# Kernel tuning notes

Measured on AMD Instinct MI355X. Metric: run time of the kernel, lower is better.

Reference implementation:

```python
import jax, jax.numpy as jnp
import numpy as np

B, CIN, COUT, H, W = 64, 64, 64, 128, 128
M1, M2 = 32, 32


def _dht(x, s=None, axes=(-2, -1)):
    # Discrete Hartley Transform: real(FFT) - imag(FFT), norm='forward'
    f = jnp.fft.fftn(x, s=s, axes=axes, norm='forward')
    return jnp.real(f) - jnp.imag(f)


def setup_inputs() -> dict:
    key = jax.random.key(0)
    k1, k2, k3 = jax.random.split(key, 3)
    scale = 1.0 / (CIN * COUT)
    x = jax.random.normal(k1, (B, CIN, H, W), dtype=jnp.float32)
    weights1 = scale * jax.random.uniform(k2, (CIN, COUT, M1, M2), dtype=jnp.float32)
    weights2 = scale * jax.random.uniform(k3, (CIN, COUT, M1, M2), dtype=jnp.float32)
    return {"x": x, "weights1": weights1, "weights2": weights2}


def reference(x, weights1, weights2):
    b = x.shape[0]  # == CIN == COUT (required for the original torch.mul broadcast)
    # Full-grid DHT over spatial dims
    x_ft = _dht(x, axes=(2, 3))  # [B, CIN, H, W]

    def spectral_block(a, w):
        # convolution_using_DHT: DHT(a) * DHT(w), then inverse = (1/len) * DHT
        prod = _dht(a, axes=(-2, -1)) * _dht(w, axes=(-2, -1))  # [B, COUT, M1, M2]
        return (1.0 / b) * _dht(prod, axes=(-2, -1))  # len(prod) = b

    c1 = spectral_block(x_ft[:, :, :M1, :M2], weights1)
    c2 = spectral_block(x_ft[:, :, -M1:, :M2], weights2)

    # out_ft is cfloat in torch but only assigned real values -> keep real
    out_ft = jnp.zeros((b, COUT, H, W // 2 + 1), dtype=jnp.float32)
    out_ft = out_ft.at[:, :, :M1, :M2].set(c1)
    out_ft = out_ft.at[:, :, -M1:, :M2].set(c2)

    # InverseDHT with s=(H, W): zero-pads last dim from W//2+1 to W, scale 1/len
    return (1.0 / b) * _dht(out_ft, s=(H, W), axes=(2, 3))  # [B, COUT, H, W]
```

## Files before the change

kernel.cpp:

```cpp
#include <hip/hip_runtime.h>


#define OFF_T3   0
#define OFF_T4T  2048
#define OFF_TF   4096
#define OFF_XCY  53248
#define WS_FLOATS (53248 + 4096 * 2048)

typedef __attribute__((ext_vector_type(8))) short bf16x8;
typedef __attribute__((ext_vector_type(4))) float f32x4;

__device__ __forceinline__ int kmap(int i) { return (i < 32) ? i : 64 + i; }

__device__ __forceinline__ unsigned short f2bf(float f) {
    unsigned int u = __float_as_uint(f);
    return (unsigned short)((u + 0x7fffu + ((u >> 16) & 1u)) >> 16);
}
__device__ __forceinline__ float bf2f(unsigned short h) {
    return __uint_as_float(((unsigned int)h) << 16);
}

__device__ __forceinline__ void fma4(float* a, float s, float4 b) {
    a[0] = fmaf(s, b.x, a[0]); a[1] = fmaf(s, b.y, a[1]);
    a[2] = fmaf(s, b.z, a[2]); a[3] = fmaf(s, b.w, a[3]);
}

__global__ __launch_bounds__(256) void init_tables(float* ws) {
    int idx = blockIdx.x * 256 + threadIdx.x;
    if (idx >= 4096) return;
    const float w32 = 6.2831853071795864769f / 32.0f;
    if (idx < 2048) {
        int n2 = idx >> 6, j = idx & 63, jj = j & 31;
        float a = w32 * (float)((jj * n2) & 31);
        ws[OFF_T3 + idx] = (j < 32) ? cosf(a) : sinf(a);
    } else {
        int t = idx - 2048, m = t >> 5, k1 = t & 31;
        float v;
        if (m < 32) { float a = w32 * (float)((k1 * m) & 31); v = cosf(a) + sinf(a); }
        else { int mm = m - 32; float a = w32 * (float)((k1 * mm) & 31); v = cosf(a) - sinf(a); }
        ws[OFF_T4T + t] = v * (1.0f / 1024.0f);
    }
}

__global__ __launch_bounds__(256) void init_frag(float* ws) {
    unsigned short* tf = (unsigned short*)(ws + OFF_TF);
    int idx = blockIdx.x * 256 + threadIdx.x;
    if (idx >= 98304) return;
    const float w128 = 6.2831853071795864769f / 128.0f;
    float v;
    int hl;
    if (idx < 16384) {
        int frag = idx >> 9, lane = (idx >> 3) & 63, ii = idx & 7;
        hl = frag & 1;
        int nt = (frag >> 1) & 3, ks = frag >> 3;
        int n2 = ks * 32 + (lane >> 4) * 8 + ii;
        int j = nt * 16 + (lane & 15);
        int jj = j & 31;
        float a = w128 * (float)((jj * n2) & 127);
        v = (j < 32) ? cosf(a) : sinf(a);
    } else if (idx < 49152) {
        int t = idx - 16384;
        int frag = t >> 9, lane = (t >> 3) & 63, ii = t & 7;
        hl = frag & 1;
        int ks = (frag >> 1) & 7, mt = frag >> 4;
        int m = ks * 32 + (lane >> 4) * 8 + ii;
        int io = mt * 16 + (lane & 15);
        int k1 = kmap(io);
        if (m < 128) { float a = w128 * (float)((k1 * m) & 127); v = cosf(a) + sinf(a); }
        else { int mm = m - 128; float a = w128 * (float)((k1 * mm) & 127); v = cosf(a) - sinf(a); }
        v *= (1.0f / 16384.0f);
    } else if (idx < 81920) {
        int t = idx - 49152;
        int frag = t >> 9, lane = (t >> 3) & 63, ii = t & 7;
        hl = frag & 1;
        int nt = (frag >> 1) & 15, ks = frag >> 5;
        int j = ks * 32 + (lane >> 4) * 8 + ii;
        int r = nt * 16 + (lane & 15);
        int k1 = kmap(j);
        int p = r & 127;
        float a = w128 * (float)((p * k1) & 127);
        v = (r < 128) ? cosf(a) : sinf(a);
    } else {
        int t = idx - 81920;
        int frag = t >> 9, lane = (t >> 3) & 63, ii = t & 7;
        hl = frag & 1;
        int nt = (frag >> 1) & 7, ks = frag >> 4;
        int ms = ks * 32 + (lane >> 4) * 8 + ii;
        int q = nt * 16 + (lane & 15);
        int k2 = ms & 31;
        float a = w128 * (float)((q * k2) & 127);
        float c = cosf(a), s = sinf(a);
        const float s4 = 1.0f / 67108864.0f;
        v = ((ms < 32) ? (c + s) : (c - s)) * s4;
    }
    unsigned short h = f2bf(v);
    tf[idx] = hl ? f2bf(v - bf2f(h)) : h;
}

__global__ __launch_bounds__(256) void kA(const float* __restrict__ x, float* ws) {
    __shared__ unsigned short CSThi[64 * 136];
    __shared__ unsigned short CSTlo[64 * 136];
    const int tid  = threadIdx.x;
    const int lane = tid & 63;
    const int wv   = tid >> 6;
    const int ch   = blockIdx.x;
    const float* xg = x + ch * 16384;
    const int lr = lane & 15;
    const int lk = (lane >> 4) * 8;
    const int lq = (lane >> 4) * 4;

    const unsigned short* tf = (const unsigned short*)(ws + OFF_TF);
    const bf16x8* t1f = (const bf16x8*)tf;
    const bf16x8* t2f = (const bf16x8*)tf + 32 * 64;

    const f32x4 zero4 = {0.f, 0.f, 0.f, 0.f};

    f32x4 acc[2][4];
#pragma unroll
    for (int mt = 0; mt < 2; mt++)
#pragma unroll
        for (int nt = 0; nt < 4; nt++) acc[mt][nt] = zero4;

#pragma unroll
    for (int ks = 0; ks < 4; ks++) {
        bf16x8 ah[2], al[2];
#pragma unroll
        for (int mt = 0; mt < 2; mt++) {
            const float* src = xg + (wv * 32 + mt * 16 + lr) * 128 + ks * 32 + lk;
            float4 u0 = *(const float4*)src;
            float4 u1 = *(const float4*)(src + 4);
            float av[8] = {u0.x, u0.y, u0.z, u0.w, u1.x, u1.y, u1.z, u1.w};
#pragma unroll
            for (int i = 0; i < 8; i++) {
                unsigned short h = f2bf(av[i]);
                ah[mt][i] = (short)h;
                al[mt][i] = (short)f2bf(av[i] - bf2f(h));
            }
        }
#pragma unroll
        for (int nt = 0; nt < 4; nt++) {
            bf16x8 bh = t1f[((ks * 4 + nt) * 2 + 0) * 64 + lane];
            bf16x8 bl = t1f[((ks * 4 + nt) * 2 + 1) * 64 + lane];
#pragma unroll
            for (int mt = 0; mt < 2; mt++) {
                acc[mt][nt] = __builtin_amdgcn_mfma_f32_16x16x32_bf16(ah[mt], bh, acc[mt][nt], 0, 0, 0);
                acc[mt][nt] = __builtin_amdgcn_mfma_f32_16x16x32_bf16(ah[mt], bl, acc[mt][nt], 0, 0, 0);
                acc[mt][nt] = __builtin_amdgcn_mfma_f32_16x16x32_bf16(al[mt], bh, acc[mt][nt], 0, 0, 0);
            }
        }
    }

#pragma unroll
    for (int mt = 0; mt < 2; mt++)
#pragma unroll
        for (int nt = 0; nt < 4; nt++) {
            const int j  = nt * 16 + lr;
            const int n1 = wv * 32 + mt * 16 + lq;
            unsigned short h[4], lo[4];
#pragma unroll
            for (int r = 0; r < 4; r++) {
                float v = acc[mt][nt][r];
                h[r]  = f2bf(v);
                lo[r] = f2bf(v - bf2f(h[r]));
            }
            uint2 hv = make_uint2((unsigned int)h[0] | ((unsigned int)h[1] << 16),
                                  (unsigned int)h[2] | ((unsigned int)h[3] << 16));
            uint2 lv = make_uint2((unsigned int)lo[0] | ((unsigned int)lo[1] << 16),
                                  (unsigned int)lo[2] | ((unsigned int)lo[3] << 16));
            *(uint2*)&CSThi[j * 136 + n1] = hv;
            *(uint2*)&CSTlo[j * 136 + n1] = lv;
        }
    __syncthreads();

    f32x4 a2[2] = {zero4, zero4};
#pragma unroll
    for (int ks = 0; ks < 8; ks++) {
        bf16x8 ah = t2f[((wv * 8 + ks) * 2 + 0) * 64 + lane];
        bf16x8 al = t2f[((wv * 8 + ks) * 2 + 1) * 64 + lane];
        const int colb = (ks & 3) * 32 + lk;
        const int rofs = (ks >= 4) ? 32 : 0;
#pragma unroll
        for (int nt = 0; nt < 2; nt++) {
            const int row = nt * 16 + lr + rofs;
            bf16x8 bh = *(const bf16x8*)&CSThi[row * 136 + colb];
            bf16x8 bl = *(const bf16x8*)&CSTlo[row * 136 + colb];
            a2[nt] = __builtin_amdgcn_mfma_f32_16x16x32_bf16(ah, bh, a2[nt], 0, 0, 0);
            a2[nt] = __builtin_amdgcn_mfma_f32_16x16x32_bf16(ah, bl, a2[nt], 0, 0, 0);
            a2[nt] = __builtin_amdgcn_mfma_f32_16x16x32_bf16(al, bh, a2[nt], 0, 0, 0);
        }
    }
    float* xcg = ws + OFF_XCY + ch * 2048;
#pragma unroll
    for (int nt = 0; nt < 2; nt++)
#pragma unroll
        for (int r = 0; r < 4; r++) {
            const int io = wv * 16 + lq + r;
            xcg[io * 32 + nt * 16 + lr] = a2[nt][r];
        }
}

__global__ __launch_bounds__(128) void kB1(const float* __restrict__ w1, const float* __restrict__ w2,
                                           float* ws, float* wh) {
    __shared__ float inT[2304];
    __shared__ float G[4352];
    __shared__ float T3c[2048];
    __shared__ float T4c[2048];
    const int tid = threadIdx.x;
#pragma unroll
    for (int i = 0; i < 16; i++) {
        int t = i * 128 + tid;
        T3c[t] = ws[OFF_T3 + t];
        T4c[t] = ws[OFF_T4T + t];
    }
    float* dstp[2];
#pragma unroll
    for (int tt = 0; tt < 2; tt++) {
        int g = blockIdx.x * 2 + tt;
        const float* src; float* dst;
        if (g < 8192) {
            int ch = g >> 1, crop = g & 1;
            dst = ws + OFF_XCY + ch * 2048 + crop * 1024;
            src = dst;
        } else {
            int gw = g - 8192;
            int ch = gw >> 1, t2 = gw & 1;
            src = (t2 ? w2 : w1) + ch * 1024;
            dst = wh + gw * 1024;
        }
        dstp[tt] = dst;
#pragma unroll
        for (int i = 0; i < 8; i++) {
            int idx = i * 128 + tid;
            int rr = idx >> 5, cc = idx & 31;
            inT[tt * 1152 + cc * 36 + rr] = src[idx];
        }
    }
    __syncthreads();
    {
        const int tt = tid >> 6, l = tid & 63;
        const int n10 = (l >> 4) * 8;
        const int jj0 = (l & 15) * 4;
        float ac[8][4];
#pragma unroll
        for (int i = 0; i < 8; i++) { ac[i][0] = ac[i][1] = ac[i][2] = ac[i][3] = 0.f; }
#pragma unroll 4
        for (int k = 0; k < 32; k++) {
            float4 b  = *(const float4*)&T3c[k * 64 + jj0];
            float4 a0 = *(const float4*)&inT[tt * 1152 + k * 36 + n10];
            float4 a1 = *(const float4*)&inT[tt * 1152 + k * 36 + n10 + 4];
            fma4(ac[0], a0.x, b); fma4(ac[1], a0.y, b);
            fma4(ac[2], a0.z, b); fma4(ac[3], a0.w, b);
            fma4(ac[4], a1.x, b); fma4(ac[5], a1.y, b);
            fma4(ac[6], a1.z, b); fma4(ac[7], a1.w, b);
        }
#pragma unroll
        for (int i = 0; i < 8; i++)
            *(float4*)&G[tt * 2176 + (n10 + i) * 68 + jj0] =
                make_float4(ac[i][0], ac[i][1], ac[i][2], ac[i][3]);
    }
    __syncthreads();
    {
        const int tt = tid >> 6, l = tid & 63;
        const int k10 = (l >> 3) * 4;
        const int k20 = (l & 7) * 4;
        float ac[4][4];
#pragma unroll
        for (int i = 0; i < 4; i++) { ac[i][0] = ac[i][1] = ac[i][2] = ac[i][3] = 0.f; }
#pragma unroll 4
        for (int m = 0; m < 64; m++) {
            float4 av = *(const float4*)&T4c[m * 32 + k10];
            const int row = m & 31;
            const int col = (m < 32) ? k20 : (32 + k20);
            float4 bv = *(const float4*)&G[tt * 2176 + row * 68 + col];
            fma4(ac[0], av.x, bv); fma4(ac[1], av.y, bv);
            fma4(ac[2], av.z, bv); fma4(ac[3], av.w, bv);
        }
        float* dst = dstp[tt];
#pragma unroll
        for (int i = 0; i < 4; i++)
            *(float4*)&dst[(k10 + i) * 32 + k20] =
                make_float4(ac[i][0], ac[i][1], ac[i][2], ac[i][3]);
    }
}

__global__ __launch_bounds__(128) void kB2(float* ws, const float* __restrict__ wh) {
    __shared__ float prodT[2304];
    __shared__ float G[4352];
    __shared__ float T3c[2048];
    __shared__ float T4c[2048];
    const int tid = threadIdx.x;
    const int ch = blockIdx.x;
#pragma unroll
    for (int i = 0; i < 16; i++) {
        int t = i * 128 + tid;
        T3c[t] = ws[OFF_T3 + t];
        T4c[t] = ws[OFF_T4T + t];
    }
    float* xc = ws + OFF_XCY + ch * 2048;
    const float* whc = wh + ch * 2048;
#pragma unroll
    for (int i = 0; i < 16; i++) {
        int flat = i * 128 + tid;
        int c = flat >> 10, r = (flat >> 5) & 31, cc = flat & 31;
        prodT[c * 1152 + cc * 36 + r] = xc[flat] * whc[flat];
    }
    __syncthreads();
    {
        const int tt = tid >> 6, l = tid & 63;
        const int n10 = (l >> 4) * 8;
        const int jj0 = (l & 15) * 4;
        float ac[8][4];
#pragma unroll
        for (int i = 0; i < 8; i++) { ac[i][0] = ac[i][1] = ac[i][2] = ac[i][3] = 0.f; }
#pragma unroll 4
        for (int k = 0; k < 32; k++) {
            float4 b  = *(const float4*)&T3c[k * 64 + jj0];
            float4 a0 = *(const float4*)&prodT[tt * 1152 + k * 36 + n10];
            float4 a1 = *(const float4*)&prodT[tt * 1152 + k * 36 + n10 + 4];
            fma4(ac[0], a0.x, b); fma4(ac[1], a0.y, b);
            fma4(ac[2], a0.z, b); fma4(ac[3], a0.w, b);
            fma4(ac[4], a1.x, b); fma4(ac[5], a1.y, b);
            fma4(ac[6], a1.z, b); fma4(ac[7], a1.w, b);
        }
#pragma unroll
        for (int i = 0; i < 8; i++)
            *(float4*)&G[tt * 2176 + (n10 + i) * 68 + jj0] =
                make_float4(ac[i][0], ac[i][1], ac[i][2], ac[i][3]);
    }
    __syncthreads();
    {
        const int tt = tid >> 6, l = tid & 63;
        const int k10 = (l >> 3) * 4;
        const int k20 = (l & 7) * 4;
        float ac[4][4];
#pragma unroll
        for (int i = 0; i < 4; i++) { ac[i][0] = ac[i][1] = ac[i][2] = ac[i][3] = 0.f; }
#pragma unroll 4
        for (int m = 0; m < 64; m++) {
            float4 av = *(const float4*)&T4c[m * 32 + k10];
            const int row = m & 31;
            const int col = (m < 32) ? k20 : (32 + k20);
            float4 bv = *(const float4*)&G[tt * 2176 + row * 68 + col];
            fma4(ac[0], av.x, bv); fma4(ac[1], av.y, bv);
            fma4(ac[2], av.z, bv); fma4(ac[3], av.w, bv);
        }
        float* dst = xc + tt * 1024;
#pragma unroll
        for (int i = 0; i < 4; i++)
            *(float4*)&dst[(k10 + i) * 32 + k20] =
                make_float4(ac[i][0], ac[i][1], ac[i][2], ac[i][3]);
    }
}

__global__ __launch_bounds__(256) void kC(float* __restrict__ out, float* ws) {
    __shared__ unsigned short YThi[32 * 72];
    __shared__ unsigned short YTlo[32 * 72];
    __shared__ unsigned short WThi[128 * 72];
    __shared__ unsigned short WTlo[128 * 72];
    const int tid  = threadIdx.x;
    const int lane = tid & 63;
    const int wv   = tid >> 6;
    const int ch   = blockIdx.x;
    const int lr = lane & 15;
    const int lk = (lane >> 4) * 8;
    const int lq = (lane >> 4) * 4;
    const float* yg = ws + OFF_XCY + ch * 2048;

    const unsigned short* tf = (const unsigned short*)(ws + OFF_TF);
    const bf16x8* t5f = (const bf16x8*)tf + 6144;
    const bf16x8* t6f = (const bf16x8*)tf + 10240;

    const f32x4 zero4 = {0.f, 0.f, 0.f, 0.f};

    {
        const int base = tid * 8;
        const int j = base >> 5, k2b = base & 31;
        float4 u0 = *(const float4*)&yg[base];
        float4 u1 = *(const float4*)&yg[base + 4];
        float av[8] = {u0.x, u0.y, u0.z, u0.w, u1.x, u1.y, u1.z, u1.w};
#pragma unroll
        for (int i = 0; i < 8; i++) {
            unsigned short h = f2bf(av[i]);
            YThi[(k2b + i) * 72 + j] = h;
            YTlo[(k2b + i) * 72 + j] = f2bf(av[i] - bf2f(h));
        }
    }
    __syncthreads();

    f32x4 acc1[2][4];
#pragma unroll
    for (int mt = 0; mt < 2; mt++)
#pragma unroll
        for (int n = 0; n < 4; n++) acc1[mt][n] = zero4;
    bf16x8 yh[2][2], yl[2][2];
#pragma unroll
    for (int mt = 0; mt < 2; mt++)
#pragma unroll
        for (int ks = 0; ks < 2; ks++) {
            yh[mt][ks] = *(const bf16x8*)&YThi[(mt * 16 + lr) * 72 + ks * 32 + lk];
            yl[mt][ks] = *(const bf16x8*)&YTlo[(mt * 16 + lr) * 72 + ks * 32 + lk];
        }
#pragma unroll
    for (int ks = 0; ks < 2; ks++)
#pragma unroll
        for (int ntl = 0; ntl < 4; ntl++) {
            const int nt = wv * 4 + ntl;
            bf16x8 bh = t5f[((ks * 16 + nt) * 2 + 0) * 64 + lane];
            bf16x8 bl = t5f[((ks * 16 + nt) * 2 + 1) * 64 + lane];
#pragma unroll
            for (int mt = 0; mt < 2; mt++) {
                acc1[mt][ntl] = __builtin_amdgcn_mfma_f32_16x16x32_bf16(yh[mt][ks], bh, acc1[mt][ntl], 0, 0, 0);
                acc1[mt][ntl] = __builtin_amdgcn_mfma_f32_16x16x32_bf16(yh[mt][ks], bl, acc1[mt][ntl], 0, 0, 0);
                acc1[mt][ntl] = __builtin_amdgcn_mfma_f32_16x16x32_bf16(yl[mt][ks], bh, acc1[mt][ntl], 0, 0, 0);
            }
        }

#pragma unroll
    for (int mt = 0; mt < 2; mt++)
#pragma unroll
        for (int ntl = 0; ntl < 4; ntl++) {
            const int nt = wv * 4 + ntl;
            const int p = (nt & 7) * 16 + lr;
            const int ms0 = ((nt >= 8) ? 32 : 0) + mt * 16 + lq;
            unsigned short h[4], lo[4];
#pragma unroll
            for (int r = 0; r < 4; r++) {
                float v = acc1[mt][ntl][r];
                h[r]  = f2bf(v);
                lo[r] = f2bf(v - bf2f(h[r]));
            }
            *(uint2*)&WThi[p * 72 + ms0] =
                make_uint2((unsigned int)h[0] | ((unsigned int)h[1] << 16),
                           (unsigned int)h[2] | ((unsigned int)h[3] << 16));
            *(uint2*)&WTlo[p * 72 + ms0] =
                make_uint2((unsigned int)lo[0] | ((unsigned int)lo[1] << 16),
                           (unsigned int)lo[2] | ((unsigned int)lo[3] << 16));
        }
    __syncthreads();

    bf16x8 wth[2][2], wtl[2][2];
#pragma unroll
    for (int mtl = 0; mtl < 2; mtl++)
#pragma unroll
        for (int ks = 0; ks < 2; ks++) {
            const int row = (wv * 2 + mtl) * 16 + lr;
            wth[mtl][ks] = *(const bf16x8*)&WThi[row * 72 + ks * 32 + lk];
            wtl[mtl][ks] = *(const bf16x8*)&WTlo[row * 72 + ks * 32 + lk];
        }
    f32x4 acc2[2][8];
#pragma unroll
    for (int mtl = 0; mtl < 2; mtl++)
#pragma unroll
        for (int n = 0; n < 8; n++) acc2[mtl][n] = zero4;
#pragma unroll
    for (int ks = 0; ks < 2; ks++)
#pragma unroll
        for (int nt = 0; nt < 8; nt++) {
            bf16x8 bh = t6f[((ks * 8 + nt) * 2 + 0) * 64 + lane];
            bf16x8 bl = t6f[((ks * 8 + nt) * 2 + 1) * 64 + lane];
#pragma unroll
            for (int mtl = 0; mtl < 2; mtl++) {
                acc2[mtl][nt] = __builtin_amdgcn_mfma_f32_16x16x32_bf16(wth[mtl][ks], bh, acc2[mtl][nt], 0, 0, 0);
                acc2[mtl][nt] = __builtin_amdgcn_mfma_f32_16x16x32_bf16(wth[mtl][ks], bl, acc2[mtl][nt], 0, 0, 0);
                acc2[mtl][nt] = __builtin_amdgcn_mfma_f32_16x16x32_bf16(wtl[mtl][ks], bh, acc2[mtl][nt], 0, 0, 0);
            }
        }
    float* og = out + ch * 16384;
#pragma unroll
    for (int mtl = 0; mtl < 2; mtl++) {
        const int pb = (wv * 2 + mtl) * 16 + lq;
#pragma unroll
        for (int nt = 0; nt < 8; nt++)
#pragma unroll
            for (int r = 0; r < 4; r++)
                og[(pb + r) * 128 + nt * 16 + lr] = acc2[mtl][nt][r];
    }
}

extern "C" void kernel_launch(void* const* d_in, const int* in_sizes, int n_in,
                              void* d_out, int out_size, void* d_ws, size_t ws_size,
                              hipStream_t stream) {
    (void)in_sizes; (void)n_in; (void)out_size;
    if (ws_size < (size_t)WS_FLOATS * sizeof(float)) return;
    const float* x  = (const float*)d_in[0];
    const float* w1 = (const float*)d_in[1];
    const float* w2 = (const float*)d_in[2];
    float* out = (float*)d_out;
    float* ws  = (float*)d_ws;
    float* wh  = out;

    hipLaunchKernelGGL(init_tables, dim3(16), dim3(256), 0, stream, ws);
    hipLaunchKernelGGL(init_frag, dim3(384), dim3(256), 0, stream, ws);
    hipLaunchKernelGGL(kA,  dim3(4096), dim3(256), 0, stream, x, ws);
    hipLaunchKernelGGL(kB1, dim3(8192), dim3(128), 0, stream, w1, w2, ws, wh);
    hipLaunchKernelGGL(kB2, dim3(4096), dim3(128), 0, stream, ws, wh);
    hipLaunchKernelGGL(kC,  dim3(4096), dim3(256), 0, stream, out, ws);
}
```

Before: 635.6 us.

## Fuse all spectral stages into a single per-channel kernel with MFMA 32-point DHTs

Merges the separate forward-DHT, small 32x32 spectral-block, and inverse-DHT kernels into one kernel per channel that keeps intermediates in shared memory. The fp32 CUDA-core 32-point transforms are replaced by split-bf16 MFMA matmuls using new precomputed fragment tables. This removes the large global workspace round-trip and several launches, at the cost of higher shared memory use (60KB per block), which may lower occupancy.

```diff
diff --git a/kernel.cpp b/kernel.cpp
--- a/kernel.cpp
+++ b/kernel.cpp
@@ -1,11 +1,7 @@
 #include <hip/hip_runtime.h>
 
 
-#define OFF_T3   0
-#define OFF_T4T  2048
-#define OFF_TF   4096
-#define OFF_XCY  53248
-#define WS_FLOATS (53248 + 4096 * 2048)
+#define WS_FLOATS 53248
 
 typedef __attribute__((ext_vector_type(8))) short bf16x8;
 typedef __attribute__((ext_vector_type(4))) float f32x4;
@@ -20,33 +16,25 @@
     return __uint_as_float(((unsigned int)h) << 16);
 }
 
-__device__ __forceinline__ void fma4(float* a, float s, float4 b) {
-    a[0] = fmaf(s, b.x, a[0]); a[1] = fmaf(s, b.y, a[1]);
-    a[2] = fmaf(s, b.z, a[2]); a[3] = fmaf(s, b.w, a[3]);
-}
-
-__global__ __launch_bounds__(256) void init_tables(float* ws) {
+__device__ __forceinline__ void pack4(f32x4 v, uint2* hv, uint2* lv) {
+    unsigned short h[4], lo[4];
+#pragma unroll
+    for (int r = 0; r < 4; r++) {
+        h[r]  = f2bf(v[r]);
+        lo[r] = f2bf(v[r] - bf2f(h[r]));
+    }
+    *hv = make_uint2((unsigned int)h[0] | ((unsigned int)h[1] << 16),
+                     (unsigned int)h[2] | ((unsigned int)h[3] << 16));
+    *lv = make_uint2((unsigned int)lo[0] | ((unsigned int)lo[1] << 16),
+                     (unsigned int)lo[2] | ((unsigned int)lo[3] << 16));
+}
+
+__global__ __launch_bounds__(256) void init_frag(float* ws) {
+    unsigned short* tf = (unsigned short*)ws;
     int idx = blockIdx.x * 256 + threadIdx.x;
-    if (idx >= 4096) return;
-    const float w32 = 6.2831853071795864769f / 32.0f;
-    if (idx < 2048) {
-        int n2 = idx >> 6, j = idx & 63, jj = j & 31;
-        float a = w32 * (float)((jj * n2) & 31);
-        ws[OFF_T3 + idx] = (j < 32) ? cosf(a) : sinf(a);
-    } else {
-        int t = idx - 2048, m = t >> 5, k1 = t & 31;
-        float v;
-        if (m < 32) { float a = w32 * (float)((k1 * m) & 31); v = cosf(a) + sinf(a); }
-        else { int mm = m - 32; float a = w32 * (float)((k1 * mm) & 31); v = cosf(a) - sinf(a); }
-        ws[OFF_T4T + t] = v * (1.0f / 1024.0f);
-    }
-}
-
-__global__ __launch_bounds__(256) void init_frag(float* ws) {
-    unsigned short* tf = (unsigned short*)(ws + OFF_TF);
-    int idx = blockIdx.x * 256 + threadIdx.x;
-    if (idx >= 98304) return;
+    if (idx >= 106496) return;
     const float w128 = 6.2831853071795864769f / 128.0f;
+    const float w32  = 6.2831853071795864769f / 32.0f;
     float v;
     int hl;
     if (idx < 16384) {
@@ -80,7 +68,7 @@
         int p = r & 127;
         float a = w128 * (float)((p * k1) & 127);
         v = (r < 128) ? cosf(a) : sinf(a);
-    } else {
+    } else if (idx < 98304) {
         int t = idx - 81920;
         int frag = t >> 9, lane = (t >> 3) & 63, ii = t & 7;
         hl = frag & 1;
@@ -92,84 +80,107 @@
         float c = cosf(a), s = sinf(a);
         const float s4 = 1.0f / 67108864.0f;
         v = ((ms < 32) ? (c + s) : (c - s)) * s4;
+    } else if (idx < 102400) {
+        int t = idx - 98304;
+        int frag = t >> 9, lane = (t >> 3) & 63, ii = t & 7;
+        hl = frag & 1;
+        int nt = frag >> 1;
+        int k = (lane >> 4) * 8 + ii;
+        int j = nt * 16 + (lane & 15);
+        int jj = j & 31;
+        float a = w32 * (float)((jj * k) & 31);
+        v = (j < 32) ? cosf(a) : sinf(a);
+    } else {
+        int t = idx - 102400;
+        int frag = t >> 9, lane = (t >> 3) & 63, ii = t & 7;
+        hl = frag & 1;
+        int ks = (frag >> 1) & 1, mt = frag >> 2;
+        int m = ks * 32 + (lane >> 4) * 8 + ii;
+        int k1 = mt * 16 + (lane & 15);
+        if (m < 32) { float a = w32 * (float)((k1 * m) & 31); v = cosf(a) + sinf(a); }
+        else { int mm = m - 32; float a = w32 * (float)((k1 * mm) & 31); v = cosf(a) - sinf(a); }
+        v *= (1.0f / 1024.0f);
     }
     unsigned short h = f2bf(v);
     tf[idx] = hl ? f2bf(v - bf2f(h)) : h;
 }
 
-__global__ __launch_bounds__(256) void kA(const float* __restrict__ x, float* ws) {
-    __shared__ unsigned short CSThi[64 * 136];
-    __shared__ unsigned short CSTlo[64 * 136];
+__global__ __launch_bounds__(256) void kFused(const float* __restrict__ x,
+                                              const float* __restrict__ w1,
+                                              const float* __restrict__ w2,
+                                              float* __restrict__ out,
+                                              const float* __restrict__ ws) {
+    __shared__ __align__(16) unsigned char smem[61440];
     const int tid  = threadIdx.x;
     const int lane = tid & 63;
     const int wv   = tid >> 6;
     const int ch   = blockIdx.x;
-    const float* xg = x + ch * 16384;
     const int lr = lane & 15;
     const int lk = (lane >> 4) * 8;
     const int lq = (lane >> 4) * 4;
-
-    const unsigned short* tf = (const unsigned short*)(ws + OFF_TF);
-    const bf16x8* t1f = (const bf16x8*)tf;
-    const bf16x8* t2f = (const bf16x8*)tf + 32 * 64;
+    const float* xg = x + ch * 16384;
+
+    const bf16x8* tfv = (const bf16x8*)ws;
+    const bf16x8* t1f = tfv;
+    const bf16x8* t2f = tfv + 32 * 64;
+    const bf16x8* t5f = tfv + 96 * 64;
+    const bf16x8* t6f = tfv + 160 * 64;
+    const bf16x8* t3f = tfv + 192 * 64;
+    const bf16x8* t4f = tfv + 200 * 64;
+
+    float4 wl1 = *(const float4*)(w1 + ch * 1024 + tid * 4);
+    float4 wl2 = *(const float4*)(w2 + ch * 1024 + tid * 4);
 
     const f32x4 zero4 = {0.f, 0.f, 0.f, 0.f};
 
-    f32x4 acc[2][4];
-#pragma unroll
-    for (int mt = 0; mt < 2; mt++)
-#pragma unroll
-        for (int nt = 0; nt < 4; nt++) acc[mt][nt] = zero4;
-
-#pragma unroll
-    for (int ks = 0; ks < 4; ks++) {
-        bf16x8 ah[2], al[2];
-#pragma unroll
-        for (int mt = 0; mt < 2; mt++) {
-            const float* src = xg + (wv * 32 + mt * 16 + lr) * 128 + ks * 32 + lk;
-            float4 u0 = *(const float4*)src;
-            float4 u1 = *(const float4*)(src + 4);
-            float av[8] = {u0.x, u0.y, u0.z, u0.w, u1.x, u1.y, u1.z, u1.w};
-#pragma unroll
-            for (int i = 0; i < 8; i++) {
-                unsigned short h = f2bf(av[i]);
-                ah[mt][i] = (short)h;
-                al[mt][i] = (short)f2bf(av[i] - bf2f(h));
-            }
-        }
-#pragma unroll
-        for (int nt = 0; nt < 4; nt++) {
-            bf16x8 bh = t1f[((ks * 4 + nt) * 2 + 0) * 64 + lane];
-            bf16x8 bl = t1f[((ks * 4 + nt) * 2 + 1) * 64 + lane];
+    unsigned short* CSThi = (unsigned short*)smem;
+    unsigned short* CSTlo = (unsigned short*)(smem + 17408);
+    {
+        f32x4 acc[2][4];
+#pragma unroll
+        for (int mt = 0; mt < 2; mt++)
+#pragma unroll
+            for (int nt = 0; nt < 4; nt++) acc[mt][nt] = zero4;
+#pragma unroll
+        for (int ks = 0; ks < 4; ks++) {
+            bf16x8 ah[2], al[2];
 #pragma unroll
             for (int mt = 0; mt < 2; mt++) {
-                acc[mt][nt] = __builtin_amdgcn_mfma_f32_16x16x32_bf16(ah[mt], bh, acc[mt][nt], 0, 0, 0);
-                acc[mt][nt] = __builtin_amdgcn_mfma_f32_16x16x32_bf16(ah[mt], bl, acc[mt][nt], 0, 0, 0);
-                acc[mt][nt] = __builtin_amdgcn_mfma_f32_16x16x32_bf16(al[mt], bh, acc[mt][nt], 0, 0, 0);
-            }
-        }
-    }
-
-#pragma unroll
-    for (int mt = 0; mt < 2; mt++)
-#pragma unroll
-        for (int nt = 0; nt < 4; nt++) {
-            const int j  = nt * 16 + lr;
-            const int n1 = wv * 32 + mt * 16 + lq;
-            unsigned short h[4], lo[4];
-#pragma unroll
-            for (int r = 0; r < 4; r++) {
-                float v = acc[mt][nt][r];
-                h[r]  = f2bf(v);
-                lo[r] = f2bf(v - bf2f(h[r]));
-            }
-            uint2 hv = make_uint2((unsigned int)h[0] | ((unsigned int)h[1] << 16),
-                                  (unsigned int)h[2] | ((unsigned int)h[3] << 16));
-            uint2 lv = make_uint2((unsigned int)lo[0] | ((unsigned int)lo[1] << 16),
-                                  (unsigned int)lo[2] | ((unsigned int)lo[3] << 16));
-            *(uint2*)&CSThi[j * 136 + n1] = hv;
-            *(uint2*)&CSTlo[j * 136 + n1] = lv;
-        }
+                const float* src = xg + (wv * 32 + mt * 16 + lr) * 128 + ks * 32 + lk;
+                float4 u0 = *(const float4*)src;
+                float4 u1 = *(const float4*)(src + 4);
+                float av[8] = {u0.x, u0.y, u0.z, u0.w, u1.x, u1.y, u1.z, u1.w};
+#pragma unroll
+                for (int i = 0; i < 8; i++) {
+                    unsigned short h = f2bf(av[i]);
+                    ah[mt][i] = (short)h;
+                    al[mt][i] = (short)f2bf(av[i] - bf2f(h));
+                }
+            }
+#pragma unroll
+            for (int nt = 0; nt < 4; nt++) {
+                bf16x8 bh = t1f[((ks * 4 + nt) * 2 + 0) * 64 + lane];
+                bf16x8 bl = t1f[((ks * 4 + nt) * 2 + 1) * 64 + lane];
+#pragma unroll
+                for (int mt = 0; mt < 2; mt++) {
+                    acc[mt][nt] = __builtin_amdgcn_mfma_f32_16x16x32_bf16(ah[mt], bh, acc[mt][nt], 0, 0, 0);
+                    acc[mt][nt] = __builtin_amdgcn_mfma_f32_16x16x32_bf16(ah[mt], bl, acc[mt][nt], 0, 0, 0);
+                    acc[mt][nt] = __builtin_amdgcn_mfma_f32_16x16x32_bf16(al[mt], bh, acc[mt][nt], 0, 0, 0);
+                }
+            }
+        }
+#pragma unroll
+        for (int mt = 0; mt < 2; mt++)
+#pragma unroll
+            for (int nt = 0; nt < 4; nt++) {
+                const int j  = nt * 16 + lr;
+                const int n1 = wv * 32 + mt * 16 + lq;
+                uint2 hv, lv;
+                pack4(acc[mt][nt], &hv, &lv);
+                *(uint2*)&CSThi[j * 136 + n1] = hv;
+                *(uint2*)&CSTlo[j * 136 + n1] = lv;
+            }
+    }
     __syncthreads();
 
     f32x4 a2[2] = {zero4, zero4};
@@ -189,291 +200,277 @@
             a2[nt] = __builtin_amdgcn_mfma_f32_16x16x32_bf16(al, bh, a2[nt], 0, 0, 0);
         }
     }
-    float* xcg = ws + OFF_XCY + ch * 2048;
-#pragma unroll
-    for (int nt = 0; nt < 2; nt++)
-#pragma unroll
-        for (int r = 0; r < 4; r++) {
-            const int io = wv * 16 + lq + r;
-            xcg[io * 32 + nt * 16 + lr] = a2[nt][r];
-        }
-}
-
-__global__ __launch_bounds__(128) void kB1(const float* __restrict__ w1, const float* __restrict__ w2,
-                                           float* ws, float* wh) {
-    __shared__ float inT[2304];
-    __shared__ float G[4352];
-    __shared__ float T3c[2048];
-    __shared__ float T4c[2048];
-    const int tid = threadIdx.x;
-#pragma unroll
-    for (int i = 0; i < 16; i++) {
-        int t = i * 128 + tid;
-        T3c[t] = ws[OFF_T3 + t];
-        T4c[t] = ws[OFF_T4T + t];
-    }
-    float* dstp[2];
-#pragma unroll
-    for (int tt = 0; tt < 2; tt++) {
-        int g = blockIdx.x * 2 + tt;
-        const float* src; float* dst;
-        if (g < 8192) {
-            int ch = g >> 1, crop = g & 1;
-            dst = ws + OFF_XCY + ch * 2048 + crop * 1024;
-            src = dst;
-        } else {
-            int gw = g - 8192;
-            int ch = gw >> 1, t2 = gw & 1;
-            src = (t2 ? w2 : w1) + ch * 1024;
-            dst = wh + gw * 1024;
-        }
-        dstp[tt] = dst;
+    __syncthreads();
+
+    unsigned short* XCFhi = (unsigned short*)smem;
+    unsigned short* XCFlo = (unsigned short*)(smem + 10240);
+    {
+        const int c  = wv >> 1;
+        const int nb = (wv & 1) * 16 + lq;
+#pragma unroll
+        for (int nt = 0; nt < 2; nt++)
+#pragma unroll
+            for (int r = 0; r < 4; r++) {
+                float v = a2[nt][r];
+                unsigned short h = f2bf(v);
+                XCFhi[c * 1280 + (nb + r) * 40 + nt * 16 + lr] = h;
+                XCFlo[c * 1280 + (nb + r) * 40 + nt * 16 + lr] = f2bf(v - bf2f(h));
+            }
+        const int rw = tid >> 3, cw = (tid & 7) * 4;
+        float a1v[4] = {wl1.x, wl1.y, wl1.z, wl1.w};
+        float a2v[4] = {wl2.x, wl2.y, wl2.z, wl2.w};
+        unsigned short h1[4], l1[4], h2[4], l2[4];
+#pragma unroll
+        for (int i = 0; i < 4; i++) {
+            h1[i] = f2bf(a1v[i]); l1[i] = f2bf(a1v[i] - bf2f(h1[i]));
+            h2[i] = f2bf(a2v[i]); l2[i] = f2bf(a2v[i] - bf2f(h2[i]));
+        }
+        *(uint2*)&XCFhi[2 * 1280 + rw * 40 + cw] =
+            make_uint2((unsigned int)h1[0] | ((unsigned int)h1[1] << 16),
+                       (unsigned int)h1[2] | ((unsigned int)h1[3] << 16));
+        *(uint2*)&XCFlo[2 * 1280 + rw * 40 + cw] =
+            make_uint2((unsigned int)l1[0] | ((unsigned int)l1[1] << 16),
+                       (unsigned int)l1[2] | ((unsigned int)l1[3] << 16));
+        *(uint2*)&XCFhi[3 * 1280 + rw * 40 + cw] =
+            make_uint2((unsigned int)h2[0] | ((unsigned int)h2[1] << 16),
+                       (unsigned int)h2[2] | ((unsigned int)h2[3] << 16));
+        *(uint2*)&XCFlo[3 * 1280 + rw * 40 + cw] =
+            make_uint2((unsigned int)l2[0] | ((unsigned int)l2[1] << 16),
+                       (unsigned int)l2[2] | ((unsigned int)l2[3] << 16));
+    }
+    __syncthreads();
+
+    unsigned short* GThi = (unsigned short*)(smem + 20480);
+    unsigned short* GTlo = (unsigned short*)(smem + 40960);
+    {
+        const int t = wv;
+        f32x4 g[2][4];
+#pragma unroll
+        for (int mt = 0; mt < 2; mt++)
+#pragma unroll
+            for (int nt = 0; nt < 4; nt++) g[mt][nt] = zero4;
+        bf16x8 ah[2], al[2];
+#pragma unroll
+        for (int mt = 0; mt < 2; mt++) {
+            ah[mt] = *(const bf16x8*)&XCFhi[t * 1280 + (mt * 16 + lr) * 40 + lk];
+            al[mt] = *(const bf16x8*)&XCFlo[t * 1280 + (mt * 16 + lr) * 40 + lk];
+        }
+#pragma unroll
+        for (int nt = 0; nt < 4; nt++) {
+            bf16x8 bh = t3f[(nt * 2 + 0) * 64 + lane];
+            bf16x8 bl = t3f[(nt * 2 + 1) * 64 + lane];
+#pragma unroll
+            for (int mt = 0; mt < 2; mt++) {
+                g[mt][nt] = __builtin_amdgcn_mfma_f32_16x16x32_bf16(ah[mt], bh, g[mt][nt], 0, 0, 0);
+                g[mt][nt] = __builtin_amdgcn_mfma_f32_16x16x32_bf16(ah[mt], bl, g[mt][nt], 0, 0, 0);
+                g[mt][nt] = __builtin_amdgcn_mfma_f32_16x16x32_bf16(al[mt], bh, g[mt][nt], 0, 0, 0);
+            }
+        }
+#pragma unroll
+        for (int mt = 0; mt < 2; mt++)
+#pragma unroll
+            for (int nt = 0; nt < 4; nt++) {
+                const int j = nt * 16 + lr, n1b = mt * 16 + lq;
+                uint2 hv, lv;
+                pack4(g[mt][nt], &hv, &lv);
+                *(uint2*)&GThi[t * 2560 + j * 40 + n1b] = hv;
+                *(uint2*)&GTlo[t * 2560 + j * 40 + n1b] = lv;
+            }
+    }
+    __syncthreads();
+
+    float* HAT = (float*)smem;
+    {
+        const int t = wv;
+        f32x4 hacc[2][2];
+#pragma unroll
+        for (int mt = 0; mt < 2; mt++)
+#pragma unroll
+            for (int nt = 0; nt < 2; nt++) hacc[mt][nt] = zero4;
+#pragma unroll
+        for (int ks = 0; ks < 2; ks++) {
+#pragma unroll
+            for (int mt = 0; mt < 2; mt++) {
+                bf16x8 ah = t4f[((mt * 2 + ks) * 2 + 0) * 64 + lane];
+                bf16x8 al = t4f[((mt * 2 + ks) * 2 + 1) * 64 + lane];
+#pragma unroll
+                for (int nt = 0; nt < 2; nt++) {
+                    const int row = nt * 16 + lr + 32 * ks;
+                    bf16x8 bh = *(const bf16x8*)&GThi[t * 2560 + row * 40 + lk];
+                    bf16x8 bl = *(const bf16x8*)&GTlo[t * 2560 + row * 40 + lk];
+                    hacc[mt][nt] = __builtin_amdgcn_mfma_f32_16x16x32_bf16(ah, bh, hacc[mt][nt], 0, 0, 0);
+                    hacc[mt][nt] = __builtin_amdgcn_mfma_f32_16x16x32_bf16(ah, bl, hacc[mt][nt], 0, 0, 0);
+                    hacc[mt][nt] = __builtin_amdgcn_mfma_f32_16x16x32_bf16(al, bh, hacc[mt][nt], 0, 0, 0);
+                }
+            }
+        }
+        __syncthreads();
+#pragma unroll
+        for (int mt = 0; mt < 2; mt++)
+#pragma unroll
+            for (int nt = 0; nt < 2; nt++)
+#pragma unroll
+                for (int r = 0; r < 4; r++)
+                    HAT[t * 1152 + (mt * 16 + lq + r) * 36 + nt * 16 + lr] = hacc[mt][nt][r];
+    }
+    __syncthreads();
+
+    unsigned short* GT2hi = (unsigned short*)(smem + 20480);
+    unsigned short* GT2lo = (unsigned short*)(smem + 30720);
+    {
+        const int t = wv >> 1, h = wv & 1;
+        const int n1 = h * 16 + lr;
+        float pv[8];
 #pragma unroll
         for (int i = 0; i < 8; i++) {
-            int idx = i * 128 + tid;
-            int rr = idx >> 5, cc = idx & 31;
-            inT[tt * 1152 + cc * 36 + rr] = src[idx];
-        }
-    }
-    __syncthreads();
-    {
-        const int tt = tid >> 6, l = tid & 63;
-        const int n10 = (l >> 4) * 8;
-        const int jj0 = (l & 15) * 4;
-        float ac[8][4];
-#pragma unroll
-        for (int i = 0; i < 8; i++) { ac[i][0] = ac[i][1] = ac[i][2] = ac[i][3] = 0.f; }
-#pragma unroll 4
-        for (int k = 0; k < 32; k++) {
-            float4 b  = *(const float4*)&T3c[k * 64 + jj0];
-            float4 a0 = *(const float4*)&inT[tt * 1152 + k * 36 + n10];
-            float4 a1 = *(const float4*)&inT[tt * 1152 + k * 36 + n10 + 4];
-            fma4(ac[0], a0.x, b); fma4(ac[1], a0.y, b);
-            fma4(ac[2], a0.z, b); fma4(ac[3], a0.w, b);
-            fma4(ac[4], a1.x, b); fma4(ac[5], a1.y, b);
-            fma4(ac[6], a1.z, b); fma4(ac[7], a1.w, b);
-        }
-#pragma unroll
-        for (int i = 0; i < 8; i++)
-            *(float4*)&G[tt * 2176 + (n10 + i) * 68 + jj0] =
-                make_float4(ac[i][0], ac[i][1], ac[i][2], ac[i][3]);
-    }
-    __syncthreads();
-    {
-        const int tt = tid >> 6, l = tid & 63;
-        const int k10 = (l >> 3) * 4;
-        const int k20 = (l & 7) * 4;
-        float ac[4][4];
-#pragma unroll
-        for (int i = 0; i < 4; i++) { ac[i][0] = ac[i][1] = ac[i][2] = ac[i][3] = 0.f; }
-#pragma unroll 4
-        for (int m = 0; m < 64; m++) {
-            float4 av = *(const float4*)&T4c[m * 32 + k10];
-            const int row = m & 31;
-            const int col = (m < 32) ? k20 : (32 + k20);
-            float4 bv = *(const float4*)&G[tt * 2176 + row * 68 + col];
-            fma4(ac[0], av.x, bv); fma4(ac[1], av.y, bv);
-            fma4(ac[2], av.z, bv); fma4(ac[3], av.w, bv);
-        }
-        float* dst = dstp[tt];
-#pragma unroll
-        for (int i = 0; i < 4; i++)
-            *(float4*)&dst[(k10 + i) * 32 + k20] =
-                make_float4(ac[i][0], ac[i][1], ac[i][2], ac[i][3]);
-    }
-}
-
-__global__ __launch_bounds__(128) void kB2(float* ws, const float* __restrict__ wh) {
-    __shared__ float prodT[2304];
-    __shared__ float G[4352];
-    __shared__ float T3c[2048];
-    __shared__ float T4c[2048];
-    const int tid = threadIdx.x;
-    const int ch = blockIdx.x;
-#pragma unroll
-    for (int i = 0; i < 16; i++) {
-        int t = i * 128 + tid;
-        T3c[t] = ws[OFF_T3 + t];
-        T4c[t] = ws[OFF_T4T + t];
-    }
-    float* xc = ws + OFF_XCY + ch * 2048;
-    const float* whc = wh + ch * 2048;
-#pragma unroll
-    for (int i = 0; i < 16; i++) {
-        int flat = i * 128 + tid;
-        int c = flat >> 10, r = (flat >> 5) & 31, cc = flat & 31;
-        prodT[c * 1152 + cc * 36 + r] = xc[flat] * whc[flat];
-    }
-    __syncthreads();
-    {
-        const int tt = tid >> 6, l = tid & 63;
-        const int n10 = (l >> 4) * 8;
-        const int jj0 = (l & 15) * 4;
-        float ac[8][4];
-#pragma unroll
-        for (int i = 0; i < 8; i++) { ac[i][0] = ac[i][1] = ac[i][2] = ac[i][3] = 0.f; }
-#pragma unroll 4
-        for (int k = 0; k < 32; k++) {
-            float4 b  = *(const float4*)&T3c[k * 64 + jj0];
-            float4 a0 = *(const float4*)&prodT[tt * 1152 + k * 36 + n10];
-            float4 a1 = *(const float4*)&prodT[tt * 1152 + k * 36 + n10 + 4];
-            fma4(ac[0], a0.x, b); fma4(ac[1], a0.y, b);
-            fma4(ac[2], a0.z, b); fma4(ac[3], a0.w, b);
-            fma4(ac[4], a1.x, b); fma4(ac[5], a1.y, b);
-            fma4(ac[6], a1.z, b); fma4(ac[7], a1.w, b);
-        }
-#pragma unroll
-        for (int i = 0; i < 8; i++)
-            *(float4*)&G[tt * 2176 + (n10 + i) * 68 + jj0] =
-                make_float4(ac[i][0], ac[i][1], ac[i][2], ac[i][3]);
-    }
-    __syncthreads();
-    {
-        const int tt = tid >> 6, l = tid & 63;
-        const int k10 = (l >> 3) * 4;
-        const int k20 = (l & 7) * 4;
-        float ac[4][4];
-#pragma unroll
-        for (int i = 0; i < 4; i++) { ac[i][0] = ac[i][1] = ac[i][2] = ac[i][3] = 0.f; }
-#pragma unroll 4
-        for (int m = 0; m < 64; m++) {
-            float4 av = *(const float4*)&T4c[m * 32 + k10];
-            const int row = m & 31;
-            const int col = (m < 32) ? k20 : (32 + k20);
-            float4 bv = *(const float4*)&G[tt * 2176 + row * 68 + col];
-            fma4(ac[0], av.x, bv); fma4(ac[1], av.y, bv);
-            fma4(ac[2], av.z, bv); fma4(ac[3], av.w, bv);
-        }
-        float* dst = xc + tt * 1024;
-#pragma unroll
-        for (int i = 0; i < 4; i++)
-            *(float4*)&dst[(k10 + i) * 32 + k20] =
-                make_float4(ac[i][0], ac[i][1], ac[i][2], ac[i][3]);
-    }
-}
-
-__global__ __launch_bounds__(256) void kC(float* __restrict__ out, float* ws) {
-    __shared__ unsigned short YThi[32 * 72];
-    __shared__ unsigned short YTlo[32 * 72];
-    __shared__ unsigned short WThi[128 * 72];
-    __shared__ unsigned short WTlo[128 * 72];
-    const int tid  = threadIdx.x;
-    const int lane = tid & 63;
-    const int wv   = tid >> 6;
-    const int ch   = blockIdx.x;
-    const int lr = lane & 15;
-    const int lk = (lane >> 4) * 8;
-    const int lq = (lane >> 4) * 4;
-    const float* yg = ws + OFF_XCY + ch * 2048;
-
-    const unsigned short* tf = (const unsigned short*)(ws + OFF_TF);
-    const bf16x8* t5f = (const bf16x8*)tf + 6144;
-    const bf16x8* t6f = (const bf16x8*)tf + 10240;
-
-    const f32x4 zero4 = {0.f, 0.f, 0.f, 0.f};
-
-    {
-        const int base = tid * 8;
-        const int j = base >> 5, k2b = base & 31;
-        float4 u0 = *(const float4*)&yg[base];
-        float4 u1 = *(const float4*)&yg[base + 4];
-        float av[8] = {u0.x, u0.y, u0.z, u0.w, u1.x, u1.y, u1.z, u1.w};
+            float px = HAT[t * 1152 + n1 * 36 + lk + i];
+            float pw = HAT[(t + 2) * 1152 + n1 * 36 + lk + i];
+            pv[i] = px * pw;
+        }
+        bf16x8 ah, al;
 #pragma unroll
         for (int i = 0; i < 8; i++) {
-            unsigned short h = f2bf(av[i]);
-            YThi[(k2b + i) * 72 + j] = h;
-            YTlo[(k2b + i) * 72 + j] = f2bf(av[i] - bf2f(h));
-        }
-    }
-    __syncthreads();
-
-    f32x4 acc1[2][4];
-#pragma unroll
-    for (int mt = 0; mt < 2; mt++)
-#pragma unroll
-        for (int n = 0; n < 4; n++) acc1[mt][n] = zero4;
-    bf16x8 yh[2][2], yl[2][2];
-#pragma unroll
-    for (int mt = 0; mt < 2; mt++)
+            unsigned short hh = f2bf(pv[i]);
+            ah[i] = (short)hh;
+            al[i] = (short)f2bf(pv[i] - bf2f(hh));
+        }
+        f32x4 g[4];
+#pragma unroll
+        for (int nt = 0; nt < 4; nt++) g[nt] = zero4;
+#pragma unroll
+        for (int nt = 0; nt < 4; nt++) {
+            bf16x8 bh = t3f[(nt * 2 + 0) * 64 + lane];
+            bf16x8 bl = t3f[(nt * 2 + 1) * 64 + lane];
+            g[nt] = __builtin_amdgcn_mfma_f32_16x16x32_bf16(ah, bh, g[nt], 0, 0, 0);
+            g[nt] = __builtin_amdgcn_mfma_f32_16x16x32_bf16(ah, bl, g[nt], 0, 0, 0);
+            g[nt] = __builtin_amdgcn_mfma_f32_16x16x32_bf16(al, bh, g[nt], 0, 0, 0);
+        }
+#pragma unroll
+        for (int nt = 0; nt < 4; nt++) {
+            const int j = nt * 16 + lr, n1b = h * 16 + lq;
+            uint2 hv, lv;
+            pack4(g[nt], &hv, &lv);
+            *(uint2*)&GT2hi[t * 2560 + j * 40 + n1b] = hv;
+            *(uint2*)&GT2lo[t * 2560 + j * 40 + n1b] = lv;
+        }
+    }
+    __syncthreads();
+
+    unsigned short* YThi = (unsigned short*)smem;
+    unsigned short* YTlo = (unsigned short*)(smem + 4608);
+    {
+        const int t = wv >> 1, h = wv & 1;
+        f32x4 ya[2] = {zero4, zero4};
 #pragma unroll
         for (int ks = 0; ks < 2; ks++) {
-            yh[mt][ks] = *(const bf16x8*)&YThi[(mt * 16 + lr) * 72 + ks * 32 + lk];
-            yl[mt][ks] = *(const bf16x8*)&YTlo[(mt * 16 + lr) * 72 + ks * 32 + lk];
-        }
-#pragma unroll
-    for (int ks = 0; ks < 2; ks++)
-#pragma unroll
-        for (int ntl = 0; ntl < 4; ntl++) {
-            const int nt = wv * 4 + ntl;
-            bf16x8 bh = t5f[((ks * 16 + nt) * 2 + 0) * 64 + lane];
-            bf16x8 bl = t5f[((ks * 16 + nt) * 2 + 1) * 64 + lane];
-#pragma unroll
-            for (int mt = 0; mt < 2; mt++) {
-                acc1[mt][ntl] = __builtin_amdgcn_mfma_f32_16x16x32_bf16(yh[mt][ks], bh, acc1[mt][ntl], 0, 0, 0);
-                acc1[mt][ntl] = __builtin_amdgcn_mfma_f32_16x16x32_bf16(yh[mt][ks], bl, acc1[mt][ntl], 0, 0, 0);
-                acc1[mt][ntl] = __builtin_amdgcn_mfma_f32_16x16x32_bf16(yl[mt][ks], bh, acc1[mt][ntl], 0, 0, 0);
-            }
-        }
-
-#pragma unroll
-    for (int mt = 0; mt < 2; mt++)
-#pragma unroll
-        for (int ntl = 0; ntl < 4; ntl++) {
-            const int nt = wv * 4 + ntl;
-            const int p = (nt & 7) * 16 + lr;
-            const int ms0 = ((nt >= 8) ? 32 : 0) + mt * 16 + lq;
-            unsigned short h[4], lo[4];
-#pragma unroll
-            for (int r = 0; r < 4; r++) {
-                float v = acc1[mt][ntl][r];
-                h[r]  = f2bf(v);
-                lo[r] = f2bf(v - bf2f(h[r]));
-            }
-            *(uint2*)&WThi[p * 72 + ms0] =
-                make_uint2((unsigned int)h[0] | ((unsigned int)h[1] << 16),
-                           (unsigned int)h[2] | ((unsigned int)h[3] << 16));
-            *(uint2*)&WTlo[p * 72 + ms0] =
-                make_uint2((unsigned int)lo[0] | ((unsigned int)lo[1] << 16),
-                           (unsigned int)lo[2] | ((unsigned int)lo[3] << 16));
-        }
-    __syncthreads();
-
-    bf16x8 wth[2][2], wtl[2][2];
-#pragma unroll
-    for (int mtl = 0; mtl < 2; mtl++)
-#pragma unroll
-        for (int ks = 0; ks < 2; ks++) {
-            const int row = (wv * 2 + mtl) * 16 + lr;
-            wth[mtl][ks] = *(const bf16x8*)&WThi[row * 72 + ks * 32 + lk];
-            wtl[mtl][ks] = *(const bf16x8*)&WTlo[row * 72 + ks * 32 + lk];
-        }
-    f32x4 acc2[2][8];
-#pragma unroll
-    for (int mtl = 0; mtl < 2; mtl++)
-#pragma unroll
-        for (int n = 0; n < 8; n++) acc2[mtl][n] = zero4;
-#pragma unroll
-    for (int ks = 0; ks < 2; ks++)
-#pragma unroll
-        for (int nt = 0; nt < 8; nt++) {
-            bf16x8 bh = t6f[((ks * 8 + nt) * 2 + 0) * 64 + lane];
-            bf16x8 bl = t6f[((ks * 8 + nt) * 2 + 1) * 64 + lane];
-#pragma unroll
-            for (int mtl = 0; mtl < 2; mtl++) {
-                acc2[mtl][nt] = __builtin_amdgcn_mfma_f32_16x16x32_bf16(wth[mtl][ks], bh, acc2[mtl][nt], 0, 0, 0);
-                acc2[mtl][nt] = __builtin_amdgcn_mfma_f32_16x16x32_bf16(wth[mtl][ks], bl, acc2[mtl][nt], 0, 0, 0);
-                acc2[mtl][nt] = __builtin_amdgcn_mfma_f32_16x16x32_bf16(wtl[mtl][ks], bh, acc2[mtl][nt], 0, 0, 0);
-            }
-        }
-    float* og = out + ch * 16384;
-#pragma unroll
-    for (int mtl = 0; mtl < 2; mtl++) {
-        const int pb = (wv * 2 + mtl) * 16 + lq;
-#pragma unroll
-        for (int nt = 0; nt < 8; nt++)
-#pragma unroll
-            for (int r = 0; r < 4; r++)
-                og[(pb + r) * 128 + nt * 16 + lr] = acc2[mtl][nt][r];
+            bf16x8 ah = t4f[((h * 2 + ks) * 2 + 0) * 64 + lane];
+            bf16x8 al = t4f[((h * 2 + ks) * 2 + 1) * 64 + lane];
+#pragma unroll
+            for (int nt = 0; nt < 2; nt++) {
+                const int row = nt * 16 + lr + 32 * ks;
+                bf16x8 bh = *(const bf16x8*)&GT2hi[t * 2560 + row * 40 + lk];
+                bf16x8 bl = *(const bf16x8*)&GT2lo[t * 2560 + row * 40 + lk];
+                ya[nt] = __builtin_amdgcn_mfma_f32_16x16x32_bf16(ah, bh, ya[nt], 0, 0, 0);
+                ya[nt] = __builtin_amdgcn_mfma_f32_16x16x32_bf16(ah, bl, ya[nt], 0, 0, 0);
+                ya[nt] = __builtin_amdgcn_mfma_f32_16x16x32_bf16(al, bh, ya[nt], 0, 0, 0);
+            }
+        }
+        __syncthreads();
+#pragma unroll
+        for (int nt = 0; nt < 2; nt++) {
+            const int k2 = nt * 16 + lr;
+            const int j0 = t * 32 + h * 16 + lq;
+            uint2 hv, lv;
+            pack4(ya[nt], &hv, &lv);
+            *(uint2*)&YThi[k2 * 72 + j0] = hv;
+            *(uint2*)&YTlo[k2 * 72 + j0] = lv;
+        }
+    }
+    __syncthreads();
+
+    unsigned short* WThi = (unsigned short*)(smem + 9216);
+    unsigned short* WTlo = (unsigned short*)(smem + 27648);
+    {
+        f32x4 acc1[2][4];
+#pragma unroll
+        for (int mt = 0; mt < 2; mt++)
+#pragma unroll
+            for (int n = 0; n < 4; n++) acc1[mt][n] = zero4;
+        bf16x8 yh[2][2], yl[2][2];
+#pragma unroll
+        for (int mt = 0; mt < 2; mt++)
+#pragma unroll
+            for (int ks = 0; ks < 2; ks++) {
+                yh[mt][ks] = *(const bf16x8*)&YThi[(mt * 16 + lr) * 72 + ks * 32 + lk];
+                yl[mt][ks] = *(const bf16x8*)&YTlo[(mt * 16 + lr) * 72 + ks * 32 + lk];
+            }
+#pragma unroll
+        for (int ks = 0; ks < 2; ks++)
+#pragma unroll
+            for (int ntl = 0; ntl < 4; ntl++) {
+                const int nt = wv * 4 + ntl;
+                bf16x8 bh = t5f[((ks * 16 + nt) * 2 + 0) * 64 + lane];
+                bf16x8 bl = t5f[((ks * 16 + nt) * 2 + 1) * 64 + lane];
+#pragma unroll
+                for (int mt = 0; mt < 2; mt++) {
+                    acc1[mt][ntl] = __builtin_amdgcn_mfma_f32_16x16x32_bf16(yh[mt][ks], bh, acc1[mt][ntl], 0, 0, 0);
+                    acc1[mt][ntl] = __builtin_amdgcn_mfma_f32_16x16x32_bf16(yh[mt][ks], bl, acc1[mt][ntl], 0, 0, 0);
+                    acc1[mt][ntl] = __builtin_amdgcn_mfma_f32_16x16x32_bf16(yl[mt][ks], bh, acc1[mt][ntl], 0, 0, 0);
+                }
+            }
+#pragma unroll
+        for (int mt = 0; mt < 2; mt++)
+#pragma unroll
+            for (int ntl = 0; ntl < 4; ntl++) {
+                const int nt = wv * 4 + ntl;
+                const int p = (nt & 7) * 16 + lr;
+                const int ms0 = ((nt >= 8) ? 32 : 0) + mt * 16 + lq;
+                uint2 hv, lv;
+                pack4(acc1[mt][ntl], &hv, &lv);
+                *(uint2*)&WThi[p * 72 + ms0] = hv;
+                *(uint2*)&WTlo[p * 72 + ms0] = lv;
+            }
+    }
+    __syncthreads();
+
+    {
+        bf16x8 wth[2][2], wtl[2][2];
+#pragma unroll
+        for (int mtl = 0; mtl < 2; mtl++)
+#pragma unroll
+            for (int ks = 0; ks < 2; ks++) {
+                const int row = (wv * 2 + mtl) * 16 + lr;
+                wth[mtl][ks] = *(const bf16x8*)&WThi[row * 72 + ks * 32 + lk];
+                wtl[mtl][ks] = *(const bf16x8*)&WTlo[row * 72 + ks * 32 + lk];
+            }
+        f32x4 acc2[2][8];
+#pragma unroll
+        for (int mtl = 0; mtl < 2; mtl++)
+#pragma unroll
+            for (int n = 0; n < 8; n++) acc2[mtl][n] = zero4;
+#pragma unroll
+        for (int ks = 0; ks < 2; ks++)
+#pragma unroll
+            for (int nt = 0; nt < 8; nt++) {
+                bf16x8 bh = t6f[((ks * 8 + nt) * 2 + 0) * 64 + lane];
+                bf16x8 bl = t6f[((ks * 8 + nt) * 2 + 1) * 64 + lane];
+#pragma unroll
+                for (int mtl = 0; mtl < 2; mtl++) {
+                    acc2[mtl][nt] = __builtin_amdgcn_mfma_f32_16x16x32_bf16(wth[mtl][ks], bh, acc2[mtl][nt], 0, 0, 0);
+                    acc2[mtl][nt] = __builtin_amdgcn_mfma_f32_16x16x32_bf16(wth[mtl][ks], bl, acc2[mtl][nt], 0, 0, 0);
+                    acc2[mtl][nt] = __builtin_amdgcn_mfma_f32_16x16x32_bf16(wtl[mtl][ks], bh, acc2[mtl][nt], 0, 0, 0);
+                }
+            }
+        float* og = out + ch * 16384;
+#pragma unroll
+        for (int mtl = 0; mtl < 2; mtl++) {
+            const int pb = (wv * 2 + mtl) * 16 + lq;
+#pragma unroll
+            for (int nt = 0; nt < 8; nt++)
+#pragma unroll
+                for (int r = 0; r < 4; r++)
+                    og[(pb + r) * 128 + nt * 16 + lr] = acc2[mtl][nt][r];
+        }
     }
 }
 
@@ -487,12 +484,7 @@
     const float* w2 = (const float*)d_in[2];
     float* out = (float*)d_out;
     float* ws  = (float*)d_ws;
-    float* wh  = out;
-
-    hipLaunchKernelGGL(init_tables, dim3(16), dim3(256), 0, stream, ws);
-    hipLaunchKernelGGL(init_frag, dim3(384), dim3(256), 0, stream, ws);
-    hipLaunchKernelGGL(kA,  dim3(4096), dim3(256), 0, stream, x, ws);
-    hipLaunchKernelGGL(kB1, dim3(8192), dim3(128), 0, stream, w1, w2, ws, wh);
-    hipLaunchKernelGGL(kB2, dim3(4096), dim3(128), 0, stream, ws, wh);
-    hipLaunchKernelGGL(kC,  dim3(4096), dim3(256), 0, stream, out, ws);
-}
+
+    hipLaunchKernelGGL(init_frag, dim3(416), dim3(256), 0, stream, ws);
+    hipLaunchKernelGGL(kFused, dim3(4096), dim3(256), 0, stream, x, w1, w2, out, ws);
+}
```

Result: faster. 557.3 us (-12.3%).
